# Kernel optimization log

Measured on AMD Instinct MI355X. Metric: run time of the kernel, lower is better.

The kernel has to match this reference:

```python
import jax, jax.numpy as jnp
import numpy as np

H = 16          # num_heads
MAX_SCALE_MUL = float(np.log(100.0))
EPS = 1e-12     # F.normalize eps


def setup_inputs() -> dict:
    key = jax.random.key(0)
    ks = jax.random.split(key, 8)
    B, L, C = 8, 1024, 1024
    x = jax.random.normal(ks[0], (B, L, C), dtype=jnp.float32)
    attn_bias = jax.random.normal(ks[1], (1, H, L, L), dtype=jnp.float32) * 0.1
    w_qkv = jax.random.normal(ks[2], (3 * C, C), dtype=jnp.float32) * (C ** -0.5)
    q_bias = jnp.zeros((C,), dtype=jnp.float32)
    v_bias = jnp.zeros((C,), dtype=jnp.float32)
    scale_mul = jnp.full((1, H, 1, 1), np.log(4.0), dtype=jnp.float32)
    w_proj = jax.random.normal(ks[3], (C, C), dtype=jnp.float32) * (C ** -0.5)
    b_proj = jnp.zeros((C,), dtype=jnp.float32)
    return dict(x=x, attn_bias=attn_bias, w_qkv=w_qkv, q_bias=q_bias,
                v_bias=v_bias, scale_mul=scale_mul, w_proj=w_proj, b_proj=b_proj)


def _l2norm(t):
    # matches F.normalize(dim=-1): t / max(||t||_2, eps)
    n = jnp.sqrt(jnp.sum(t * t, axis=-1, keepdims=True))
    return t / jnp.maximum(n, EPS)


def reference(x, attn_bias, w_qkv, q_bias, v_bias, scale_mul, w_proj, b_proj):
    B, L, C = x.shape
    D = C // H
    bias = jnp.concatenate([q_bias, jnp.zeros_like(q_bias), v_bias])
    qkv = x @ w_qkv.T + bias                      # [B,L,3C]
    qkv = qkv.reshape(B, L, 3, H, D).transpose(2, 0, 3, 1, 4)  # [3,B,H,L,D]
    q, k, v = qkv[0], qkv[1], qkv[2]
    sm = jnp.exp(jnp.minimum(scale_mul, MAX_SCALE_MUL))        # [1,H,1,1]
    q = _l2norm(q) * sm
    k = _l2norm(k)
    attn = jnp.einsum('bhld,bhmd->bhlm', q, k) + attn_bias     # scale == 1
    attn = jax.nn.softmax(attn, axis=-1)
    out = jnp.einsum('bhlm,bhmd->bhld', attn, v)               # [B,H,L,D]
    out = out.transpose(0, 2, 1, 3).reshape(B, L, C)
    return out @ w_proj.T + b_proj
```

## Files before the change

kernel.cpp:

```cpp
#include <hip/hip_runtime.h>
#include <hip/hip_bf16.h>


#define LN100 4.6051701859880914f

typedef __attribute__((ext_vector_type(8))) short short8;
typedef __attribute__((ext_vector_type(4))) float f32x4;
typedef __attribute__((ext_vector_type(4))) unsigned int u32x4;

#define MFMA_BF16(a, b, c) __builtin_amdgcn_mfma_f32_16x16x32_bf16(a, b, c, 0, 0, 0)

__device__ __forceinline__ unsigned short f2bf(float f) {
  unsigned u = __float_as_uint(f);
  u += 0x7fffu + ((u >> 16) & 1u);
  return (unsigned short)(u >> 16);
}
__device__ __forceinline__ float bf2f(unsigned short h) {
  return __uint_as_float(((unsigned)h) << 16);
}
__device__ __forceinline__ unsigned int pkbf2(float a, float b) {
  union { __hip_bfloat162 t; unsigned int u; } c;
  c.t = __float22bfloat162_rn(make_float2(a, b));
  return c.u;
}

__device__ __forceinline__ float bias_sel0(const float* qb, const float* vb, int col) {
  if (col < 1024) return qb[col];
  if (col < 2048) return 0.0f;
  return vb[col - 2048];
}

#define G2L16(gp, lp) __builtin_amdgcn_global_load_lds( \
    (const __attribute__((address_space(1))) void*)(gp), \
    (__attribute__((address_space(3))) void*)(lp), 16, 0, 0)

__global__ __launch_bounds__(256)
void split_f32_bf16(const float* __restrict__ in, unsigned short* __restrict__ hi,
                    unsigned short* __restrict__ lo, int n4)
{
  int i = blockIdx.x * blockDim.x + threadIdx.x;
  if (i >= n4) return;
  float4 v = ((const float4*)in)[i];
  ushort4 h, l;
  h.x = f2bf(v.x); l.x = f2bf(v.x - bf2f(h.x));
  h.y = f2bf(v.y); l.y = f2bf(v.y - bf2f(h.y));
  h.z = f2bf(v.z); l.z = f2bf(v.z - bf2f(h.z));
  h.w = f2bf(v.w); l.w = f2bf(v.w - bf2f(h.w));
  ((ushort4*)hi)[i] = h;
  ((ushort4*)lo)[i] = l;
}

template <int MODE>
__global__ __launch_bounds__(256)
void gemm_nt_split(const unsigned short* __restrict__ Ah, const unsigned short* __restrict__ Al,
                   const unsigned short* __restrict__ Wh, const unsigned short* __restrict__ Wl,
                   const float* __restrict__ b0, const float* __restrict__ b1,
                   float* __restrict__ C,
                   unsigned short* __restrict__ vth, unsigned short* __restrict__ vtl,
                   int M, int N, int K)
{
  __shared__ unsigned short sA[128 * 64];
  __shared__ unsigned short sW[128 * 64];

  const int tid  = threadIdx.x;
  const int lane = tid & 63;
  const int l15  = lane & 15, lg = lane >> 4;
  const int w    = tid >> 6;
  const int wr   = (w >> 1) << 6;
  const int wc   = (w & 1) << 6;
  const int m0   = blockIdx.y << 7;
  const int n0   = blockIdx.x << 7;

  f32x4 acc[4][4];
  #pragma unroll
  for (int i = 0; i < 4; ++i)
    #pragma unroll
    for (int j = 0; j < 4; ++j)
      acc[i][j] = (f32x4){0.f, 0.f, 0.f, 0.f};

  for (int k0 = 0; k0 < K; k0 += 32) {
    __syncthreads();
    #pragma unroll
    for (int u = 0; u < 4; ++u) {
      int idx = (u << 8) + tid;
      int row = idx >> 3;
      int c   = idx & 7;
      int s   = c ^ (row & 7);
      size_t rbA = (size_t)(m0 + row) * K + k0;
      size_t rbW = (size_t)(n0 + row) * K + k0;
      const unsigned short* srcA = (s < 4) ? (Ah + rbA + (s << 3))
                                           : (Al + rbA + ((s - 4) << 3));
      const unsigned short* srcW = (s < 4) ? (Wh + rbW + (s << 3))
                                           : (Wl + rbW + ((s - 4) << 3));
      G2L16(srcA, sA + (idx << 3));
      G2L16(srcW, sW + (idx << 3));
    }
    __syncthreads();

    short8 ah[4], al[4];
    #pragma unroll
    for (int i = 0; i < 4; ++i) {
      int row = wr + (i << 4) + l15;
      ah[i] = *(const short8*)(sA + (row << 6) + ((lg       ^ (row & 7)) << 3));
      al[i] = *(const short8*)(sA + (row << 6) + (((4 + lg) ^ (row & 7)) << 3));
    }
    #pragma unroll
    for (int j = 0; j < 4; ++j) {
      int row = wc + (j << 4) + l15;
      short8 wh = *(const short8*)(sW + (row << 6) + ((lg       ^ (row & 7)) << 3));
      short8 wl = *(const short8*)(sW + (row << 6) + (((4 + lg) ^ (row & 7)) << 3));
      #pragma unroll
      for (int i = 0; i < 4; ++i) {
        acc[i][j] = MFMA_BF16(ah[i], wh, acc[i][j]);
        acc[i][j] = MFMA_BF16(ah[i], wl, acc[i][j]);
        acc[i][j] = MFMA_BF16(al[i], wh, acc[i][j]);
      }
    }
  }

  if (MODE == 0 && n0 >= 2048) {
    #pragma unroll
    for (int j = 0; j < 4; ++j) {
      int col = n0 + wc + (j << 4) + l15;
      int d   = col - 2048;
      int hh  = d >> 6, dd = d & 63;
      float bb = b1[d];
      #pragma unroll
      for (int i = 0; i < 4; ++i) {
        int row  = m0 + wr + (i << 4) + (lg << 2);
        int bidx = row >> 10;
        int l    = row & 1023;
        int cbase = (((l >> 4) & 1) << 2) + (((l >> 2) & 3) << 3) + ((l >> 5) << 5);
        size_t obase = ((((size_t)bidx << 4) + hh) << 6) + dd;
        obase = obase * 1024 + cbase;
        ushort4 hv, lv;
        float v0 = acc[i][j][0] + bb;
        float v1 = acc[i][j][1] + bb;
        float v2 = acc[i][j][2] + bb;
        float v3 = acc[i][j][3] + bb;
        hv.x = f2bf(v0); lv.x = f2bf(v0 - bf2f(hv.x));
        hv.y = f2bf(v1); lv.y = f2bf(v1 - bf2f(hv.y));
        hv.z = f2bf(v2); lv.z = f2bf(v2 - bf2f(hv.z));
        hv.w = f2bf(v3); lv.w = f2bf(v3 - bf2f(hv.w));
        *(ushort4*)(vth + obase) = hv;
        *(ushort4*)(vtl + obase) = lv;
      }
    }
  } else {
    #pragma unroll
    for (int j = 0; j < 4; ++j) {
      int col = n0 + wc + (j << 4) + l15;
      float bb = (MODE == 1) ? b0[col] : bias_sel0(b0, b1, col);
      #pragma unroll
      for (int i = 0; i < 4; ++i) {
        int rbase = m0 + wr + (i << 4) + (lg << 2);
        #pragma unroll
        for (int r = 0; r < 4; ++r)
          C[(size_t)(rbase + r) * N + col] = acc[i][j][r] + bb;
      }
    }
  }
}

__global__ __launch_bounds__(256)
void qk_norm_split(const float* __restrict__ qkv, const float* __restrict__ scale_mul,
                   unsigned short* __restrict__ qk_h, unsigned short* __restrict__ qk_l)
{
  int wave = (blockIdx.x << 2) + (threadIdx.x >> 6);
  int lane = threadIdx.x & 63;
  int h  = wave & 15;
  int bl = wave >> 4;
  size_t base = (size_t)bl * 3072 + (h << 6) + lane;
  float q = qkv[base];
  float k = qkv[base + 1024];
  float sq = q * q, sk = k * k;
  #pragma unroll
  for (int off = 32; off; off >>= 1) {
    sq += __shfl_xor(sq, off);
    sk += __shfl_xor(sk, off);
  }
  float sm = __expf(fminf(scale_mul[h], LN100));
  q = q / fmaxf(sqrtf(sq), 1e-12f) * sm;
  k = k / fmaxf(sqrtf(sk), 1e-12f);
  size_t ob = (size_t)bl * 2048 + (h << 6) + lane;
  unsigned short qh = f2bf(q);
  qk_h[ob] = qh;          qk_l[ob] = f2bf(q - bf2f(qh));
  unsigned short kh = f2bf(k);
  qk_h[ob + 1024] = kh;   qk_l[ob + 1024] = f2bf(k - bf2f(kh));
}

__global__ __launch_bounds__(256, 2)
void attn_mfma(const unsigned short* __restrict__ qk_h, const unsigned short* __restrict__ qk_l,
               const unsigned short* __restrict__ vth, const unsigned short* __restrict__ vtl,
               const float* __restrict__ bias,
               unsigned short* __restrict__ oh, unsigned short* __restrict__ ol)
{
  __shared__ unsigned short sKh[4096], sKl[4096];
  __shared__ unsigned short sVh[4096], sVl[4096];

  const int tid  = threadIdx.x;
  const int lane = tid & 63;
  const int l15  = lane & 15, lg = lane >> 4;
  const int w    = tid >> 6;
  const int qt = blockIdx.x & 7;
  const int h  = (blockIdx.x >> 3) & 15;
  const int b  = blockIdx.x >> 7;
  const int q0 = qt << 7;

  short8 qh[2][2], qlo[2][2];
  #pragma unroll
  for (int qf = 0; qf < 2; ++qf) {
    size_t rb = ((size_t)((b << 10) + q0 + (w << 5) + (qf << 4) + l15)) * 2048
              + (h << 6) + (lg << 3);
    qh[qf][0]  = *(const short8*)(qk_h + rb);
    qh[qf][1]  = *(const short8*)(qk_h + rb + 32);
    qlo[qf][0] = *(const short8*)(qk_l + rb);
    qlo[qf][1] = *(const short8*)(qk_l + rb + 32);
  }

  f32x4 ao[2][4];
  float mr[2], lr[2];
  #pragma unroll
  for (int qf = 0; qf < 2; ++qf) {
    #pragma unroll
    for (int j = 0; j < 4; ++j) ao[qf][j] = (f32x4){0.f, 0.f, 0.f, 0.f};
    mr[qf] = -3.0e38f; lr[qf] = 0.0f;
  }

  const unsigned short* kh_base = qk_h + 1024 + (h << 6);
  const unsigned short* kl_base = qk_l + 1024 + (h << 6);
  const size_t vbase = ((size_t)((b << 4) + h)) * 65536;
  const float* bias_base = bias + ((size_t)h << 20)
                         + (size_t)(q0 + (w << 5) + l15) * 1024 + (lg << 2);

  for (int kv0 = 0; kv0 < 1024; kv0 += 64) {
    __syncthreads();
    #pragma unroll
    for (int u = 0; u < 2; ++u) {
      int idx = (u << 8) + tid;
      int r = idx >> 3, c = idx & 7;
      int s = c ^ (r & 7);
      size_t krow = (size_t)((b << 10) + kv0 + r) * 2048 + (s << 3);
      size_t vrow = vbase + (size_t)r * 1024 + kv0 + (s << 3);
      G2L16(kh_base + krow, sKh + (idx << 3));
      G2L16(kl_base + krow, sKl + (idx << 3));
      G2L16(vth + vrow,     sVh + (idx << 3));
      G2L16(vtl + vrow,     sVl + (idx << 3));
    }
    __syncthreads();

    #pragma unroll
    for (int qf = 0; qf < 2; ++qf) {
      f32x4 sv[4];
      #pragma unroll
      for (int j = 0; j < 4; ++j) {
        float4 bv = *(const float4*)(bias_base + (size_t)(qf << 4) * 1024
                                     + kv0 + (j << 4));
        f32x4 a = (f32x4){bv.x, bv.y, bv.z, bv.w};
        int row = (j << 4) + l15;
        int c0 = lg ^ (row & 7);
        int c1 = (lg + 4) ^ (row & 7);
        short8 kh0 = *(const short8*)(sKh + (row << 6) + (c0 << 3));
        short8 kl0 = *(const short8*)(sKl + (row << 6) + (c0 << 3));
        short8 kh1 = *(const short8*)(sKh + (row << 6) + (c1 << 3));
        short8 kl1 = *(const short8*)(sKl + (row << 6) + (c1 << 3));
        a = MFMA_BF16(kh0, qh[qf][0], a);
        a = MFMA_BF16(kl0, qh[qf][0], a);
        a = MFMA_BF16(kh0, qlo[qf][0], a);
        a = MFMA_BF16(kh1, qh[qf][1], a);
        a = MFMA_BF16(kl1, qh[qf][1], a);
        a = MFMA_BF16(kh1, qlo[qf][1], a);
        sv[j] = a;
      }

      float mx = -3.0e38f;
      #pragma unroll
      for (int j = 0; j < 4; ++j)
        #pragma unroll
        for (int r = 0; r < 4; ++r) mx = fmaxf(mx, sv[j][r]);
      mx = fmaxf(mx, __shfl_xor(mx, 16));
      mx = fmaxf(mx, __shfl_xor(mx, 32));
      float mn = fmaxf(mr[qf], mx);
      float al = __expf(mr[qf] - mn);
      mr[qf] = mn;
      float rs = 0.0f;
      #pragma unroll
      for (int j = 0; j < 4; ++j)
        #pragma unroll
        for (int r = 0; r < 4; ++r) {
          float e = __expf(sv[j][r] - mn);
          sv[j][r] = e;
          rs += e;
        }
      rs += __shfl_xor(rs, 16);
      rs += __shfl_xor(rs, 32);
      lr[qf] = lr[qf] * al + rs;
      #pragma unroll
      for (int r = 0; r < 4; ++r) {
        float av = __shfl(al, (lg << 2) + r);
        #pragma unroll
        for (int jd = 0; jd < 4; ++jd) ao[qf][jd][r] *= av;
      }

      #pragma unroll
      for (int ks = 0; ks < 2; ++ks) {
        unsigned int h0 = pkbf2(sv[2*ks][0],     sv[2*ks][1]);
        unsigned int h1 = pkbf2(sv[2*ks][2],     sv[2*ks][3]);
        unsigned int h2 = pkbf2(sv[2*ks + 1][0], sv[2*ks + 1][1]);
        unsigned int h3 = pkbf2(sv[2*ks + 1][2], sv[2*ks + 1][3]);
        unsigned int l0 = pkbf2(sv[2*ks][0]     - __uint_as_float(h0 << 16),
                                sv[2*ks][1]     - __uint_as_float(h0 & 0xffff0000u));
        unsigned int l1 = pkbf2(sv[2*ks][2]     - __uint_as_float(h1 << 16),
                                sv[2*ks][3]     - __uint_as_float(h1 & 0xffff0000u));
        unsigned int l2 = pkbf2(sv[2*ks + 1][0] - __uint_as_float(h2 << 16),
                                sv[2*ks + 1][1] - __uint_as_float(h2 & 0xffff0000u));
        unsigned int l3 = pkbf2(sv[2*ks + 1][2] - __uint_as_float(h3 << 16),
                                sv[2*ks + 1][3] - __uint_as_float(h3 & 0xffff0000u));
        union { u32x4 u; short8 s; } ph, pl;
        ph.u = (u32x4){h0, h1, h2, h3};
        pl.u = (u32x4){l0, l1, l2, l3};
        #pragma unroll
        for (int jd = 0; jd < 4; ++jd) {
          int vr = (jd << 4) + l15;
          int c  = ((ks << 2) + lg) ^ (vr & 7);
          short8 vh = *(const short8*)(sVh + (vr << 6) + (c << 3));
          short8 vl = *(const short8*)(sVl + (vr << 6) + (c << 3));
          ao[qf][jd] = MFMA_BF16(ph.s, vh, ao[qf][jd]);
          ao[qf][jd] = MFMA_BF16(ph.s, vl, ao[qf][jd]);
          ao[qf][jd] = MFMA_BF16(pl.s, vh, ao[qf][jd]);
        }
      }
    }
  }

  #pragma unroll
  for (int qf = 0; qf < 2; ++qf)
    #pragma unroll
    for (int r = 0; r < 4; ++r) {
      float lv  = __shfl(lr[qf], (lg << 2) + r);
      float inv = 1.0f / lv;
      size_t orow = ((size_t)((b << 10) + q0 + (w << 5) + (qf << 4) + (lg << 2) + r)) * 1024
                  + (h << 6) + l15;
      #pragma unroll
      for (int jd = 0; jd < 4; ++jd) {
        float v = ao[qf][jd][r] * inv;
        unsigned short hb = f2bf(v);
        oh[orow + (jd << 4)] = hb;
        ol[orow + (jd << 4)] = f2bf(v - bf2f(hb));
      }
    }
}

template <int MODE>
__global__ __launch_bounds__(256)
void gemm_nt(const float* __restrict__ A, const float* __restrict__ Bw,
             const float* __restrict__ b0, const float* __restrict__ b1,
             float* __restrict__ C, int M, int N, int K)
{
  __shared__ float As[32][132];
  __shared__ float Bs[32][132];
  const int tid = threadIdx.x;
  const int tx = tid & 15, ty = tid >> 4;
  const int m0 = blockIdx.y << 7;
  const int n0 = blockIdx.x << 7;

  float acc[8][8];
  #pragma unroll
  for (int i = 0; i < 8; ++i)
    #pragma unroll
    for (int j = 0; j < 8; ++j) acc[i][j] = 0.0f;

  for (int k0 = 0; k0 < K; k0 += 32) {
    #pragma unroll
    for (int u = 0; u < 4; ++u) {
      int f   = tid + (u << 8);
      int row = f >> 3;
      int kk  = (f & 7) << 2;
      float4 av = *(const float4*)(A  + (size_t)(m0 + row) * K + k0 + kk);
      As[kk + 0][row] = av.x; As[kk + 1][row] = av.y;
      As[kk + 2][row] = av.z; As[kk + 3][row] = av.w;
      float4 bv = *(const float4*)(Bw + (size_t)(n0 + row) * K + k0 + kk);
      Bs[kk + 0][row] = bv.x; Bs[kk + 1][row] = bv.y;
      Bs[kk + 2][row] = bv.z; Bs[kk + 3][row] = bv.w;
    }
    __syncthreads();
    #pragma unroll
    for (int kk = 0; kk < 32; ++kk) {
      float a[8], bq[8];
      *(float4*)(a)      = *(const float4*)(&As[kk][(ty << 3)]);
      *(float4*)(a + 4)  = *(const float4*)(&As[kk][(ty << 3) + 4]);
      *(float4*)(bq)     = *(const float4*)(&Bs[kk][(tx << 3)]);
      *(float4*)(bq + 4) = *(const float4*)(&Bs[kk][(tx << 3) + 4]);
      #pragma unroll
      for (int i = 0; i < 8; ++i)
        #pragma unroll
        for (int j = 0; j < 8; ++j)
          acc[i][j] = fmaf(a[i], bq[j], acc[i][j]);
    }
    __syncthreads();
  }

  #pragma unroll
  for (int i = 0; i < 8; ++i) {
    int row = m0 + (ty << 3) + i;
    #pragma unroll
    for (int j4 = 0; j4 < 2; ++j4) {
      int col = n0 + (tx << 3) + (j4 << 2);
      float4 r;
      float bbv[4];
      #pragma unroll
      for (int j = 0; j < 4; ++j)
        bbv[j] = (MODE == 0) ? bias_sel0(b0, b1, col + j) : b0[col + j];
      r.x = acc[i][j4 * 4 + 0] + bbv[0];
      r.y = acc[i][j4 * 4 + 1] + bbv[1];
      r.z = acc[i][j4 * 4 + 2] + bbv[2];
      r.w = acc[i][j4 * 4 + 3] + bbv[3];
      *(float4*)(C + (size_t)row * N + col) = r;
    }
  }
}

__global__ __launch_bounds__(256)
void qk_norm(float* __restrict__ qkv, const float* __restrict__ scale_mul)
{
  int wave = (blockIdx.x << 2) + (threadIdx.x >> 6);
  int lane = threadIdx.x & 63;
  int h  = wave & 15;
  int bl = wave >> 4;
  size_t base = (size_t)bl * 3072 + (h << 6) + lane;
  float q = qkv[base];
  float k = qkv[base + 1024];
  float sq = q * q, sk = k * k;
  #pragma unroll
  for (int off = 32; off; off >>= 1) {
    sq += __shfl_xor(sq, off);
    sk += __shfl_xor(sk, off);
  }
  float sm = __expf(fminf(scale_mul[h], LN100));
  q = q / fmaxf(sqrtf(sq), 1e-12f) * sm;
  k = k / fmaxf(sqrtf(sk), 1e-12f);
  qkv[base]        = q;
  qkv[base + 1024] = k;
}

#define SW(r, c4) ((((c4) ^ ((r) >> 2)) & 15) << 2)

template <int OUTMODE>
__global__ __launch_bounds__(256)
void attn_fwd(const float* __restrict__ qkv, const float* __restrict__ bias,
              float* __restrict__ aout,
              unsigned short* __restrict__ ah, unsigned short* __restrict__ al)
{
  __shared__ float Qs[64][64];
  __shared__ float Ks[64][64];
  __shared__ float Vs[64][64];
  __shared__ float Ps[64][64];

  const int tid = threadIdx.x;
  const int tx = tid & 15, ty = tid >> 4;
  const int qt = blockIdx.x & 15;
  const int h  = (blockIdx.x >> 4) & 15;
  const int b  = blockIdx.x >> 8;
  const int q0 = qt << 6;

  #pragma unroll
  for (int u = 0; u < 4; ++u) {
    int f = tid + (u << 8);
    int r = f >> 4, c4 = f & 15;
    float4 v = *(const float4*)(qkv + (size_t)(b * 1024 + q0 + r) * 3072 + (h << 6) + (c4 << 2));
    *(float4*)(&Qs[r][SW(r, c4)]) = v;
  }

  float o[4][4];
  float mr[4], lr[4];
  #pragma unroll
  for (int i = 0; i < 4; ++i) {
    mr[i] = -3.0e38f; lr[i] = 0.0f;
    #pragma unroll
    for (int j = 0; j < 4; ++j) o[i][j] = 0.0f;
  }

  for (int kv0 = 0; kv0 < 1024; kv0 += 64) {
    __syncthreads();
    #pragma unroll
    for (int u = 0; u < 4; ++u) {
      int f = tid + (u << 8);
      int r = f >> 4, c4 = f & 15;
      size_t gb = (size_t)(b * 1024 + kv0 + r) * 3072 + (h << 6) + (c4 << 2);
      *(float4*)(&Ks[r][SW(r, c4)]) = *(const float4*)(qkv + gb + 1024);
      *(float4*)(&Vs[r][SW(r, c4)]) = *(const float4*)(qkv + gb + 2048);
    }
    __syncthreads();

    float s[4][4];
    #pragma unroll
    for (int i = 0; i < 4; ++i)
      #pragma unroll
      for (int j = 0; j < 4; ++j) s[i][j] = 0.0f;

    #pragma unroll 4
    for (int d4 = 0; d4 < 16; ++d4) {
      float4 qv[4], kv[4];
      #pragma unroll
      for (int i = 0; i < 4; ++i)
        qv[i] = *(const float4*)(&Qs[(ty << 2) + i][SW((ty << 2) + i, d4)]);
      #pragma unroll
      for (int j = 0; j < 4; ++j)
        kv[j] = *(const float4*)(&Ks[(tx << 2) + j][SW((tx << 2) + j, d4)]);
      #pragma unroll
      for (int i = 0; i < 4; ++i)
        #pragma unroll
        for (int j = 0; j < 4; ++j)
          s[i][j] += qv[i].x * kv[j].x + qv[i].y * kv[j].y +
                     qv[i].z * kv[j].z + qv[i].w * kv[j].w;
    }

    float p[4][4];
    #pragma unroll
    for (int i = 0; i < 4; ++i) {
      float4 bv = *(const float4*)(bias + (size_t)((h << 10) + q0 + (ty << 2) + i) * 1024
                                        + kv0 + (tx << 2));
      s[i][0] += bv.x; s[i][1] += bv.y; s[i][2] += bv.z; s[i][3] += bv.w;
      float mx = fmaxf(fmaxf(s[i][0], s[i][1]), fmaxf(s[i][2], s[i][3]));
      #pragma unroll
      for (int off = 1; off < 16; off <<= 1) mx = fmaxf(mx, __shfl_xor(mx, off));
      float mn = fmaxf(mr[i], mx);
      float alp = __expf(mr[i] - mn);
      float rs = 0.0f;
      #pragma unroll
      for (int j = 0; j < 4; ++j) { p[i][j] = __expf(s[i][j] - mn); rs += p[i][j]; }
      #pragma unroll
      for (int off = 1; off < 16; off <<= 1) rs += __shfl_xor(rs, off);
      lr[i] = lr[i] * alp + rs;
      mr[i] = mn;
      #pragma unroll
      for (int j = 0; j < 4; ++j) o[i][j] *= alp;
    }

    #pragma unroll
    for (int jj = 0; jj < 4; ++jj)
      #pragma unroll
      for (int i = 0; i < 4; ++i)
        Ps[(tx << 2) + jj][SW((tx << 2) + jj, ty) + i] = p[i][jj];
    __syncthreads();

    #pragma unroll 8
    for (int j = 0; j < 64; ++j) {
      float4 pv = *(const float4*)(&Ps[j][SW(j, ty)]);
      float4 vv = *(const float4*)(&Vs[j][SW(j, tx)]);
      o[0][0] += pv.x * vv.x; o[0][1] += pv.x * vv.y; o[0][2] += pv.x * vv.z; o[0][3] += pv.x * vv.w;
      o[1][0] += pv.y * vv.x; o[1][1] += pv.y * vv.y; o[1][2] += pv.y * vv.z; o[1][3] += pv.y * vv.w;
      o[2][0] += pv.z * vv.x; o[2][1] += pv.z * vv.y; o[2][2] += pv.z * vv.z; o[2][3] += pv.z * vv.w;
      o[3][0] += pv.w * vv.x; o[3][1] += pv.w * vv.y; o[3][2] += pv.w * vv.z; o[3][3] += pv.w * vv.w;
    }
  }

  #pragma unroll
  for (int i = 0; i < 4; ++i) {
    float inv = 1.0f / lr[i];
    float v0 = o[i][0] * inv, v1 = o[i][1] * inv, v2 = o[i][2] * inv, v3 = o[i][3] * inv;
    if (OUTMODE == 0) {
      float4 r; r.x = v0; r.y = v1; r.z = v2; r.w = v3;
      *(float4*)(aout + (size_t)(b * 1024 + q0 + (ty << 2) + i) * 1024 + (h << 6) + (tx << 2)) = r;
    } else {
      ushort4 hh, ll;
      hh.x = f2bf(v0); ll.x = f2bf(v0 - bf2f(hh.x));
      hh.y = f2bf(v1); ll.y = f2bf(v1 - bf2f(hh.y));
      hh.z = f2bf(v2); ll.z = f2bf(v2 - bf2f(hh.z));
      hh.w = f2bf(v3); ll.w = f2bf(v3 - bf2f(hh.w));
      size_t idx = (size_t)(b * 1024 + q0 + (ty << 2) + i) * 256 + (h << 4) + tx;
      ((ushort4*)ah)[idx] = hh;
      ((ushort4*)al)[idx] = ll;
    }
  }
}

extern "C" void kernel_launch(void* const* d_in, const int* in_sizes, int n_in,
                              void* d_out, int out_size, void* d_ws, size_t ws_size,
                              hipStream_t stream) {
  const float* x         = (const float*)d_in[0];
  const float* attn_bias = (const float*)d_in[1];
  const float* w_qkv     = (const float*)d_in[2];
  const float* q_bias    = (const float*)d_in[3];
  const float* v_bias    = (const float*)d_in[4];
  const float* scale_mul = (const float*)d_in[5];
  const float* w_proj    = (const float*)d_in[6];
  const float* b_proj    = (const float*)d_in[7];
  float* out = (float*)d_out;

  const size_t MiB = 1024 * 1024;
  char* ws = (char*)d_ws;
  dim3 blk(256);

  if (ws_size >= 240 * MiB) {
    float*          qkv = (float*)ws;
    unsigned short* xh  = (unsigned short*)(ws + 96  * MiB);
    unsigned short* xl  = (unsigned short*)(ws + 112 * MiB);
    unsigned short* qkh = (unsigned short*)(ws + 128 * MiB);
    unsigned short* qkl = (unsigned short*)(ws + 160 * MiB);
    unsigned short* vth = (unsigned short*)(ws + 192 * MiB);
    unsigned short* vtl = (unsigned short*)(ws + 208 * MiB);
    unsigned short* wqh = (unsigned short*)(ws + 224 * MiB);
    unsigned short* wql = (unsigned short*)(ws + 230 * MiB);
    unsigned short* wph = (unsigned short*)(ws + 236 * MiB);
    unsigned short* wpl = (unsigned short*)(ws + 238 * MiB);

    split_f32_bf16<<<dim3(8192), blk, 0, stream>>>(x,      xh,  xl,  2097152);
    split_f32_bf16<<<dim3(3072), blk, 0, stream>>>(w_qkv,  wqh, wql, 786432);
    split_f32_bf16<<<dim3(1024), blk, 0, stream>>>(w_proj, wph, wpl, 262144);

    gemm_nt_split<0><<<dim3(24, 64), blk, 0, stream>>>(xh, xl, wqh, wql,
        q_bias, v_bias, qkv, vth, vtl, 8192, 3072, 1024);
    qk_norm_split<<<dim3(32768), blk, 0, stream>>>(qkv, scale_mul, qkh, qkl);
    attn_mfma<<<dim3(1024), blk, 0, stream>>>(qkh, qkl, vth, vtl, attn_bias, xh, xl);
    gemm_nt_split<1><<<dim3(8, 64), blk, 0, stream>>>(xh, xl, wph, wpl,
        b_proj, nullptr, out, nullptr, nullptr, 8192, 1024, 1024);
  } else if (ws_size >= 144 * MiB) {
    float*          qkv = (float*)ws;
    unsigned short* xh  = (unsigned short*)(ws + 96  * MiB);
    unsigned short* xl  = (unsigned short*)(ws + 112 * MiB);
    unsigned short* wqh = (unsigned short*)(ws + 128 * MiB);
    unsigned short* wql = (unsigned short*)(ws + 134 * MiB);
    unsigned short* wph = (unsigned short*)(ws + 140 * MiB);
    unsigned short* wpl = (unsigned short*)(ws + 142 * MiB);

    split_f32_bf16<<<dim3(8192), blk, 0, stream>>>(x,      xh,  xl,  2097152);
    split_f32_bf16<<<dim3(3072), blk, 0, stream>>>(w_qkv,  wqh, wql, 786432);
    split_f32_bf16<<<dim3(1024), blk, 0, stream>>>(w_proj, wph, wpl, 262144);

    gemm_nt_split<2><<<dim3(24, 64), blk, 0, stream>>>(xh, xl, wqh, wql,
        q_bias, v_bias, qkv, nullptr, nullptr, 8192, 3072, 1024);
    qk_norm<<<dim3(32768), blk, 0, stream>>>(qkv, scale_mul);
    attn_fwd<1><<<dim3(2048), blk, 0, stream>>>(qkv, attn_bias, nullptr, xh, xl);
    gemm_nt_split<1><<<dim3(8, 64), blk, 0, stream>>>(xh, xl, wph, wpl,
        b_proj, nullptr, out, nullptr, nullptr, 8192, 1024, 1024);
  } else {
    float* qkv = (float*)ws;
    float* att = qkv + (size_t)8192 * 3072;
    gemm_nt<0><<<dim3(24, 64), blk, 0, stream>>>(x, w_qkv, q_bias, v_bias, qkv, 8192, 3072, 1024);
    qk_norm<<<dim3(32768), blk, 0, stream>>>(qkv, scale_mul);
    attn_fwd<0><<<dim3(2048), blk, 0, stream>>>(qkv, attn_bias, att, nullptr, nullptr);
    gemm_nt<1><<<dim3(8, 64), blk, 0, stream>>>(att, w_proj, b_proj, nullptr, out, 8192, 1024, 1024);
  }
}
```

Measured before the change: 539.1 us.

## Fuse QK L2-norm into QKV GEMM epilogue and widen attention KV tile

The QKV GEMM epilogue now computes per-head L2 norms of the Q and K columns directly from accumulators via lane shuffles, applies the scale, and writes bf16 hi/lo splits. This removes the fp32 qkv round trip and the separate qk_norm_split kernel. The attention kernel's KV tile also grows from 64 to 128 keys per sync, with a new V shared-memory swizzle, to halve barriers and load phases. The cost is doubled LDS use (64KB per block), which may cut occupancy for the two-blocks-per-CU launch bound.

```diff
diff --git a/kernel.cpp b/kernel.cpp
--- a/kernel.cpp
+++ b/kernel.cpp
@@ -55,7 +55,9 @@
 void gemm_nt_split(const unsigned short* __restrict__ Ah, const unsigned short* __restrict__ Al,
                    const unsigned short* __restrict__ Wh, const unsigned short* __restrict__ Wl,
                    const float* __restrict__ b0, const float* __restrict__ b1,
+                   const float* __restrict__ scale_mul,
                    float* __restrict__ C,
+                   unsigned short* __restrict__ qkh, unsigned short* __restrict__ qkl,
                    unsigned short* __restrict__ vth, unsigned short* __restrict__ vtl,
                    int M, int N, int K)
 {
@@ -146,6 +148,50 @@
         *(ushort4*)(vtl + obase) = lv;
       }
     }
+  } else if (MODE == 0) {
+    const int colbase = n0 + wc;
+    const int third   = colbase >> 10;
+    const int h       = (colbase >> 6) & 15;
+    const float sm    = (third == 0) ? __expf(fminf(scale_mul[h], LN100)) : 1.0f;
+    if (third == 0) {
+      #pragma unroll
+      for (int j = 0; j < 4; ++j) {
+        float bb = b0[colbase + (j << 4) + l15];
+        #pragma unroll
+        for (int i = 0; i < 4; ++i)
+          #pragma unroll
+          for (int r = 0; r < 4; ++r) acc[i][j][r] += bb;
+      }
+    }
+    float ss[4][4];
+    #pragma unroll
+    for (int i = 0; i < 4; ++i)
+      #pragma unroll
+      for (int r = 0; r < 4; ++r)
+        ss[i][r] = acc[i][0][r] * acc[i][0][r] + acc[i][1][r] * acc[i][1][r]
+                 + acc[i][2][r] * acc[i][2][r] + acc[i][3][r] * acc[i][3][r];
+    #pragma unroll
+    for (int off = 1; off < 16; off <<= 1)
+      #pragma unroll
+      for (int i = 0; i < 4; ++i)
+        #pragma unroll
+        for (int r = 0; r < 4; ++r)
+          ss[i][r] += __shfl_xor(ss[i][r], off);
+    #pragma unroll
+    for (int i = 0; i < 4; ++i)
+      #pragma unroll
+      for (int r = 0; r < 4; ++r) {
+        float inv = sm / fmaxf(sqrtf(ss[i][r]), 1e-12f);
+        int row = m0 + wr + (i << 4) + (lg << 2) + r;
+        size_t ob = (size_t)row * 2048 + (third << 10) + (h << 6) + l15;
+        #pragma unroll
+        for (int j = 0; j < 4; ++j) {
+          float v = acc[i][j][r] * inv;
+          unsigned short hb = f2bf(v);
+          qkh[ob + (j << 4)] = hb;
+          qkl[ob + (j << 4)] = f2bf(v - bf2f(hb));
+        }
+      }
   } else {
     #pragma unroll
     for (int j = 0; j < 4; ++j) {
@@ -160,33 +206,6 @@
       }
     }
   }
-}
-
-__global__ __launch_bounds__(256)
-void qk_norm_split(const float* __restrict__ qkv, const float* __restrict__ scale_mul,
-                   unsigned short* __restrict__ qk_h, unsigned short* __restrict__ qk_l)
-{
-  int wave = (blockIdx.x << 2) + (threadIdx.x >> 6);
-  int lane = threadIdx.x & 63;
-  int h  = wave & 15;
-  int bl = wave >> 4;
-  size_t base = (size_t)bl * 3072 + (h << 6) + lane;
-  float q = qkv[base];
-  float k = qkv[base + 1024];
-  float sq = q * q, sk = k * k;
-  #pragma unroll
-  for (int off = 32; off; off >>= 1) {
-    sq += __shfl_xor(sq, off);
-    sk += __shfl_xor(sk, off);
-  }
-  float sm = __expf(fminf(scale_mul[h], LN100));
-  q = q / fmaxf(sqrtf(sq), 1e-12f) * sm;
-  k = k / fmaxf(sqrtf(sk), 1e-12f);
-  size_t ob = (size_t)bl * 2048 + (h << 6) + lane;
-  unsigned short qh = f2bf(q);
-  qk_h[ob] = qh;          qk_l[ob] = f2bf(q - bf2f(qh));
-  unsigned short kh = f2bf(k);
-  qk_h[ob + 1024] = kh;   qk_l[ob + 1024] = f2bf(k - bf2f(kh));
 }
 
 __global__ __launch_bounds__(256, 2)
@@ -195,8 +214,8 @@
                const float* __restrict__ bias,
                unsigned short* __restrict__ oh, unsigned short* __restrict__ ol)
 {
-  __shared__ unsigned short sKh[4096], sKl[4096];
-  __shared__ unsigned short sVh[4096], sVl[4096];
+  __shared__ unsigned short sKh[8192], sKl[8192];
+  __shared__ unsigned short sVh[8192], sVl[8192];
 
   const int tid  = threadIdx.x;
   const int lane = tid & 63;
@@ -233,101 +252,111 @@
   const float* bias_base = bias + ((size_t)h << 20)
                          + (size_t)(q0 + (w << 5) + l15) * 1024 + (lg << 2);
 
-  for (int kv0 = 0; kv0 < 1024; kv0 += 64) {
-    __syncthreads();
-    #pragma unroll
-    for (int u = 0; u < 2; ++u) {
+  for (int kv0 = 0; kv0 < 1024; kv0 += 128) {
+    __syncthreads();
+    #pragma unroll
+    for (int u = 0; u < 4; ++u) {
       int idx = (u << 8) + tid;
-      int r = idx >> 3, c = idx & 7;
-      int s = c ^ (r & 7);
-      size_t krow = (size_t)((b << 10) + kv0 + r) * 2048 + (s << 3);
-      size_t vrow = vbase + (size_t)r * 1024 + kv0 + (s << 3);
-      G2L16(kh_base + krow, sKh + (idx << 3));
-      G2L16(kl_base + krow, sKl + (idx << 3));
-      G2L16(vth + vrow,     sVh + (idx << 3));
-      G2L16(vtl + vrow,     sVl + (idx << 3));
-    }
-    __syncthreads();
-
-    #pragma unroll
-    for (int qf = 0; qf < 2; ++qf) {
-      f32x4 sv[4];
-      #pragma unroll
-      for (int j = 0; j < 4; ++j) {
-        float4 bv = *(const float4*)(bias_base + (size_t)(qf << 4) * 1024
-                                     + kv0 + (j << 4));
-        f32x4 a = (f32x4){bv.x, bv.y, bv.z, bv.w};
-        int row = (j << 4) + l15;
-        int c0 = lg ^ (row & 7);
-        int c1 = (lg + 4) ^ (row & 7);
-        short8 kh0 = *(const short8*)(sKh + (row << 6) + (c0 << 3));
-        short8 kl0 = *(const short8*)(sKl + (row << 6) + (c0 << 3));
-        short8 kh1 = *(const short8*)(sKh + (row << 6) + (c1 << 3));
-        short8 kl1 = *(const short8*)(sKl + (row << 6) + (c1 << 3));
-        a = MFMA_BF16(kh0, qh[qf][0], a);
-        a = MFMA_BF16(kl0, qh[qf][0], a);
-        a = MFMA_BF16(kh0, qlo[qf][0], a);
-        a = MFMA_BF16(kh1, qh[qf][1], a);
-        a = MFMA_BF16(kl1, qh[qf][1], a);
-        a = MFMA_BF16(kh1, qlo[qf][1], a);
-        sv[j] = a;
-      }
-
-      float mx = -3.0e38f;
-      #pragma unroll
-      for (int j = 0; j < 4; ++j)
-        #pragma unroll
-        for (int r = 0; r < 4; ++r) mx = fmaxf(mx, sv[j][r]);
-      mx = fmaxf(mx, __shfl_xor(mx, 16));
-      mx = fmaxf(mx, __shfl_xor(mx, 32));
-      float mn = fmaxf(mr[qf], mx);
-      float al = __expf(mr[qf] - mn);
-      mr[qf] = mn;
-      float rs = 0.0f;
-      #pragma unroll
-      for (int j = 0; j < 4; ++j)
+      {
+        int r = idx >> 3, c = idx & 7;
+        int s = c ^ (r & 7);
+        size_t krow = (size_t)((b << 10) + kv0 + r) * 2048 + (s << 3);
+        G2L16(kh_base + krow, sKh + (idx << 3));
+        G2L16(kl_base + krow, sKl + (idx << 3));
+      }
+      {
+        int d = idx >> 4, cc = idx & 15;
+        int s = (cc & 8) | ((cc ^ d) & 7);
+        size_t vrow = vbase + (size_t)d * 1024 + kv0 + (s << 3);
+        G2L16(vth + vrow, sVh + (idx << 3));
+        G2L16(vtl + vrow, sVl + (idx << 3));
+      }
+    }
+    __syncthreads();
+
+    #pragma unroll
+    for (int hh = 0; hh < 2; ++hh) {
+      const int kvo = kv0 + (hh << 6);
+      #pragma unroll
+      for (int qf = 0; qf < 2; ++qf) {
+        f32x4 sv[4];
+        #pragma unroll
+        for (int j = 0; j < 4; ++j) {
+          float4 bv = *(const float4*)(bias_base + (size_t)(qf << 4) * 1024
+                                       + kvo + (j << 4));
+          f32x4 a = (f32x4){bv.x, bv.y, bv.z, bv.w};
+          int row = (hh << 6) + (j << 4) + l15;
+          int c0 = lg ^ (row & 7);
+          int c1 = (lg + 4) ^ (row & 7);
+          short8 kh0 = *(const short8*)(sKh + (row << 6) + (c0 << 3));
+          short8 kl0 = *(const short8*)(sKl + (row << 6) + (c0 << 3));
+          short8 kh1 = *(const short8*)(sKh + (row << 6) + (c1 << 3));
+          short8 kl1 = *(const short8*)(sKl + (row << 6) + (c1 << 3));
+          a = MFMA_BF16(kh0, qh[qf][0], a);
+          a = MFMA_BF16(kl0, qh[qf][0], a);
+          a = MFMA_BF16(kh0, qlo[qf][0], a);
+          a = MFMA_BF16(kh1, qh[qf][1], a);
+          a = MFMA_BF16(kl1, qh[qf][1], a);
+          a = MFMA_BF16(kh1, qlo[qf][1], a);
+          sv[j] = a;
+        }
+
+        float mx = -3.0e38f;
+        #pragma unroll
+        for (int j = 0; j < 4; ++j)
+          #pragma unroll
+          for (int r = 0; r < 4; ++r) mx = fmaxf(mx, sv[j][r]);
+        mx = fmaxf(mx, __shfl_xor(mx, 16));
+        mx = fmaxf(mx, __shfl_xor(mx, 32));
+        float mn = fmaxf(mr[qf], mx);
+        float al = __expf(mr[qf] - mn);
+        mr[qf] = mn;
+        float rs = 0.0f;
+        #pragma unroll
+        for (int j = 0; j < 4; ++j)
+          #pragma unroll
+          for (int r = 0; r < 4; ++r) {
+            float e = __expf(sv[j][r] - mn);
+            sv[j][r] = e;
+            rs += e;
+          }
+        rs += __shfl_xor(rs, 16);
+        rs += __shfl_xor(rs, 32);
+        lr[qf] = lr[qf] * al + rs;
         #pragma unroll
         for (int r = 0; r < 4; ++r) {
-          float e = __expf(sv[j][r] - mn);
-          sv[j][r] = e;
-          rs += e;
+          float av = __shfl(al, (lg << 2) + r);
+          #pragma unroll
+          for (int jd = 0; jd < 4; ++jd) ao[qf][jd][r] *= av;
         }
-      rs += __shfl_xor(rs, 16);
-      rs += __shfl_xor(rs, 32);
-      lr[qf] = lr[qf] * al + rs;
-      #pragma unroll
-      for (int r = 0; r < 4; ++r) {
-        float av = __shfl(al, (lg << 2) + r);
-        #pragma unroll
-        for (int jd = 0; jd < 4; ++jd) ao[qf][jd][r] *= av;
-      }
-
-      #pragma unroll
-      for (int ks = 0; ks < 2; ++ks) {
-        unsigned int h0 = pkbf2(sv[2*ks][0],     sv[2*ks][1]);
-        unsigned int h1 = pkbf2(sv[2*ks][2],     sv[2*ks][3]);
-        unsigned int h2 = pkbf2(sv[2*ks + 1][0], sv[2*ks + 1][1]);
-        unsigned int h3 = pkbf2(sv[2*ks + 1][2], sv[2*ks + 1][3]);
-        unsigned int l0 = pkbf2(sv[2*ks][0]     - __uint_as_float(h0 << 16),
-                                sv[2*ks][1]     - __uint_as_float(h0 & 0xffff0000u));
-        unsigned int l1 = pkbf2(sv[2*ks][2]     - __uint_as_float(h1 << 16),
-                                sv[2*ks][3]     - __uint_as_float(h1 & 0xffff0000u));
-        unsigned int l2 = pkbf2(sv[2*ks + 1][0] - __uint_as_float(h2 << 16),
-                                sv[2*ks + 1][1] - __uint_as_float(h2 & 0xffff0000u));
-        unsigned int l3 = pkbf2(sv[2*ks + 1][2] - __uint_as_float(h3 << 16),
-                                sv[2*ks + 1][3] - __uint_as_float(h3 & 0xffff0000u));
-        union { u32x4 u; short8 s; } ph, pl;
-        ph.u = (u32x4){h0, h1, h2, h3};
-        pl.u = (u32x4){l0, l1, l2, l3};
-        #pragma unroll
-        for (int jd = 0; jd < 4; ++jd) {
-          int vr = (jd << 4) + l15;
-          int c  = ((ks << 2) + lg) ^ (vr & 7);
-          short8 vh = *(const short8*)(sVh + (vr << 6) + (c << 3));
-          short8 vl = *(const short8*)(sVl + (vr << 6) + (c << 3));
-          ao[qf][jd] = MFMA_BF16(ph.s, vh, ao[qf][jd]);
-          ao[qf][jd] = MFMA_BF16(ph.s, vl, ao[qf][jd]);
-          ao[qf][jd] = MFMA_BF16(pl.s, vh, ao[qf][jd]);
+
+        #pragma unroll
+        for (int ks = 0; ks < 2; ++ks) {
+          unsigned int h0 = pkbf2(sv[2*ks][0],     sv[2*ks][1]);
+          unsigned int h1 = pkbf2(sv[2*ks][2],     sv[2*ks][3]);
+          unsigned int h2 = pkbf2(sv[2*ks + 1][0], sv[2*ks + 1][1]);
+          unsigned int h3 = pkbf2(sv[2*ks + 1][2], sv[2*ks + 1][3]);
+          unsigned int l0 = pkbf2(sv[2*ks][0]     - __uint_as_float(h0 << 16),
+                                  sv[2*ks][1]     - __uint_as_float(h0 & 0xffff0000u));
+          unsigned int l1 = pkbf2(sv[2*ks][2]     - __uint_as_float(h1 << 16),
+                                  sv[2*ks][3]     - __uint_as_float(h1 & 0xffff0000u));
+          unsigned int l2 = pkbf2(sv[2*ks + 1][0] - __uint_as_float(h2 << 16),
+                                  sv[2*ks + 1][1] - __uint_as_float(h2 & 0xffff0000u));
+          unsigned int l3 = pkbf2(sv[2*ks + 1][2] - __uint_as_float(h3 << 16),
+                                  sv[2*ks + 1][3] - __uint_as_float(h3 & 0xffff0000u));
+          union { u32x4 u; short8 s; } ph, pl;
+          ph.u = (u32x4){h0, h1, h2, h3};
+          pl.u = (u32x4){l0, l1, l2, l3};
+          #pragma unroll
+          for (int jd = 0; jd < 4; ++jd) {
+            int vr = (jd << 4) + l15;
+            int c  = (hh << 3) | (((ks << 2) + lg) ^ (vr & 7));
+            short8 vh = *(const short8*)(sVh + (vr << 7) + (c << 3));
+            short8 vl = *(const short8*)(sVl + (vr << 7) + (c << 3));
+            ao[qf][jd] = MFMA_BF16(ph.s, vh, ao[qf][jd]);
+            ao[qf][jd] = MFMA_BF16(ph.s, vl, ao[qf][jd]);
+            ao[qf][jd] = MFMA_BF16(pl.s, vh, ao[qf][jd]);
+          }
         }
       }
     }
@@ -593,7 +622,6 @@
   dim3 blk(256);
 
   if (ws_size >= 240 * MiB) {
-    float*          qkv = (float*)ws;
     unsigned short* xh  = (unsigned short*)(ws + 96  * MiB);
     unsigned short* xl  = (unsigned short*)(ws + 112 * MiB);
     unsigned short* qkh = (unsigned short*)(ws + 128 * MiB);
@@ -610,11 +638,11 @@
     split_f32_bf16<<<dim3(1024), blk, 0, stream>>>(w_proj, wph, wpl, 262144);
 
     gemm_nt_split<0><<<dim3(24, 64), blk, 0, stream>>>(xh, xl, wqh, wql,
-        q_bias, v_bias, qkv, vth, vtl, 8192, 3072, 1024);
-    qk_norm_split<<<dim3(32768), blk, 0, stream>>>(qkv, scale_mul, qkh, qkl);
+        q_bias, v_bias, scale_mul, nullptr, qkh, qkl, vth, vtl, 8192, 3072, 1024);
     attn_mfma<<<dim3(1024), blk, 0, stream>>>(qkh, qkl, vth, vtl, attn_bias, xh, xl);
     gemm_nt_split<1><<<dim3(8, 64), blk, 0, stream>>>(xh, xl, wph, wpl,
-        b_proj, nullptr, out, nullptr, nullptr, 8192, 1024, 1024);
+        b_proj, nullptr, nullptr, out, nullptr, nullptr, nullptr, nullptr,
+        8192, 1024, 1024);
   } else if (ws_size >= 144 * MiB) {
     float*          qkv = (float*)ws;
     unsigned short* xh  = (unsigned short*)(ws + 96  * MiB);
@@ -629,11 +657,13 @@
     split_f32_bf16<<<dim3(1024), blk, 0, stream>>>(w_proj, wph, wpl, 262144);
 
     gemm_nt_split<2><<<dim3(24, 64), blk, 0, stream>>>(xh, xl, wqh, wql,
-        q_bias, v_bias, qkv, nullptr, nullptr, 8192, 3072, 1024);
+        q_bias, v_bias, nullptr, qkv, nullptr, nullptr, nullptr, nullptr,
+        8192, 3072, 1024);
     qk_norm<<<dim3(32768), blk, 0, stream>>>(qkv, scale_mul);
     attn_fwd<1><<<dim3(2048), blk, 0, stream>>>(qkv, attn_bias, nullptr, xh, xl);
     gemm_nt_split<1><<<dim3(8, 64), blk, 0, stream>>>(xh, xl, wph, wpl,
-        b_proj, nullptr, out, nullptr, nullptr, 8192, 1024, 1024);
+        b_proj, nullptr, nullptr, out, nullptr, nullptr, nullptr, nullptr,
+        8192, 1024, 1024);
   } else {
     float* qkv = (float*)ws;
     float* att = qkv + (size_t)8192 * 3072;
```

New measurement: 599.2 us. 1.11x slower.
